# Performance work log

Measured on AMD Instinct MI355X. Metric: run time of the kernel, lower is better.

## Reference

```python
import jax, jax.numpy as jnp
import numpy as np

E, V, F_, B = 8192, 2048, 2048, 8
H, DEC, EDGE, META = 128, 128, 2, 4
MEMH, MEMAGG, AGGH = 256, 128, 128
IN_DIM = DEC + EDGE + META  # 134


def _incidence(idx, n):
    # dense (n, E) 0/1 incidence matrix, as used by torch.mm in the original
    return jnp.zeros((n, idx.shape[0]), jnp.float32).at[idx, jnp.arange(idx.shape[0])].set(1.0)


def setup_inputs() -> dict:
    key = jax.random.key(0)
    ks = jax.random.split(key, 32)
    var_idx = jax.random.randint(ks[0], (E,), 0, V)          # variable of each edge
    fun_idx = jax.random.randint(ks[1], (E,), 0, F_)         # clause of each edge
    batch_of_var = jax.random.randint(ks[2], (V,), 0, B)     # problem id of each variable
    variable_mask = _incidence(var_idx, V)                   # (V, E)
    function_mask = _incidence(fun_idx, F_)                  # (F, E)
    b_variable_mask = jnp.zeros((V, B), jnp.float32).at[jnp.arange(V), batch_of_var].set(1.0)

    def lin(k, i, o):
        kw, kb = jax.random.split(k)
        return (jax.random.normal(kw, (i, o), jnp.float32) * 0.05,
                jax.random.normal(kb, (o,), jnp.float32) * 0.05)

    p = {}
    for pre, k0 in (("v", 10), ("f", 20)):
        p[pre + "M1w"], p[pre + "M1b"] = lin(ks[k0], IN_DIM, MEMH)
        p[pre + "M2w"], p[pre + "M2b"] = lin(ks[k0 + 1], MEMH, MEMAGG)
        p[pre + "A1w"], p[pre + "A1b"] = lin(ks[k0 + 2], MEMAGG + EDGE, AGGH)
        p[pre + "A2w"], p[pre + "A2b"] = lin(ks[k0 + 3], AGGH, H)

    return dict(
        variable_state=jax.random.normal(ks[3], (E, H), jnp.float32),
        function_state=jax.random.normal(ks[4], (E, H), jnp.float32),
        decimator_variable_state=jax.random.normal(ks[5], (E, DEC), jnp.float32),
        decimator_function_state=jax.random.normal(ks[6], (E, DEC), jnp.float32),
        edge_feature=jax.random.normal(ks[7], (E, EDGE), jnp.float32),
        meta_data=jax.random.normal(ks[8], (B, META), jnp.float32),
        active_mask=jax.random.randint(ks[9], (B, 1), 0, 2),
        variable_mask=variable_mask, variable_mask_t=variable_mask.T,
        function_mask=function_mask, function_mask_t=function_mask.T,
        b_variable_mask=b_variable_mask,
        **p,
    )


def _aggregate(state, feature, mask, mask_t, W1, b1, W2, b2, A1, c1, A2, c2):
    # MessageAggregator (include_self_message=False, edge_mask=None)
    h = jax.nn.relu(state @ W1 + b1)       # (E, MEMH)  pre-aggregation transform
    h = h @ W2 + b2                        # (E, MEMAGG)
    agg = mask_t @ (mask @ h) - h          # node-sum broadcast back to edges, minus self message
    a = jax.nn.relu(jnp.concatenate([agg, feature], 1) @ A1 + c1)  # post-agg transform
    return a @ A2 + c2                     # (E, H)


def reference(variable_state, function_state, decimator_variable_state,
              decimator_function_state, edge_feature, meta_data, active_mask,
              variable_mask, variable_mask_t, function_mask, function_mask_t,
              b_variable_mask,
              vM1w, vM1b, vM2w, vM2b, vA1w, vA1b, vA2w, vA2b,
              fM1w, fM1b, fM2w, fM2b, fA1w, fA1b, fA2w, fA2b):
    # active mask broadcast: batch -> variables -> edges (dense mm chain as in torch)
    mask = variable_mask_t @ (b_variable_mask @ active_mask.astype(jnp.float32))  # (E, 1)
    # meta-data broadcast: batch -> variables -> edges
    graph_feat = variable_mask_t @ (b_variable_mask @ meta_data)                  # (E, META)

    dvs = jnp.concatenate([decimator_variable_state, edge_feature, graph_feat], 1)
    agg_v = _aggregate(dvs, edge_feature, variable_mask, variable_mask_t,
                       vM1w, vM1b, vM2w, vM2b, vA1w, vA1b, vA2w, vA2b)
    function_state = mask * agg_v + (1.0 - mask) * function_state  # dropout: identity (eval)

    dfs = jnp.concatenate([decimator_function_state, edge_feature, graph_feat], 1)
    agg_f = _aggregate(dfs, edge_feature, function_mask, function_mask_t,
                       fM1w, fM1b, fM2w, fM2b, fA1w, fA1b, fA2w, fA2b)
    variable_state = mask * agg_f + (1.0 - mask) * variable_state

    return (variable_state, function_state)
```

## Files before the change

kernel.cpp:

```cpp
#include <hip/hip_runtime.h>

#define E_N 8192
#define V_N 2048
#define F_N 2048
#define B_N 8
#define H_N 128
#define DEC_N 128
#define EDGE_N 2
#define META_N 4
#define IN_DIM 134
#define MEMH 256
#define MEMAGG 128
#define AGGH 128

typedef __attribute__((ext_vector_type(8))) short short8;
typedef __attribute__((ext_vector_type(4))) float f32x4;

__device__ inline unsigned short f2bf(float x) {
    unsigned u = __float_as_uint(x);
    unsigned r = (u + 0x7FFFu + ((u >> 16) & 1u)) >> 16;
    return (unsigned short)r;
}

__device__ inline short8 pack8(float4 u0, float4 u1) {
    short8 s;
    s[0] = (short)f2bf(u0.x); s[1] = (short)f2bf(u0.y);
    s[2] = (short)f2bf(u0.z); s[3] = (short)f2bf(u0.w);
    s[4] = (short)f2bf(u1.x); s[5] = (short)f2bf(u1.y);
    s[6] = (short)f2bf(u1.z); s[7] = (short)f2bf(u1.w);
    return s;
}

__device__ inline int probe4(float4 v, int c, int hit) {
    if (hit < 0) {
        if      (v.x != 0.f) hit = c;
        else if (v.y != 0.f) hit = c + 1;
        else if (v.z != 0.f) hit = c + 2;
        else if (v.w != 0.f) hit = c + 3;
    }
    return hit;
}

struct RDesc { const float* src; unsigned short* dst; int K; int N; int Kp; };
struct PrepArgs {
    const float* vmt; const float* fmt;
    int* vidx; int* fidx;
    const float* bvm; const int* active; const float* meta;
    float* emask; float* gfeat;
    float* nszero;
    RDesc d[8];
};
__constant__ const int RP_CUM[9] = {0, 160, 288, 368, 432, 592, 720, 800, 864};

__global__ __launch_bounds__(256) void k_prep(PrepArgs P) {
    int bid = blockIdx.x, tid = threadIdx.x;
    if (bid < 4096) {
        int row = bid * 4 + (tid >> 6);
        int lane = tid & 63;
        bool isVar = row < E_N;
        const float* m = isVar ? P.vmt : P.fmt;
        int* out = isVar ? P.vidx : P.fidx;
        int e = isVar ? row : row - E_N;
        const float4* rp = (const float4*)(m + (size_t)e * V_N);

        int hit = -1;
        float4 a0 = rp[lane], a1 = rp[64 + lane];
        hit = probe4(a0, lane * 4, hit);
        hit = probe4(a1, (64 + lane) * 4, hit);
        unsigned long long bm = __ballot(hit >= 0);
        for (int base = 128; base < 512 && !bm; base += 128) {
            float4 v0 = rp[base + lane], v1 = rp[base + 64 + lane];
            hit = probe4(v0, (base + lane) * 4, hit);
            hit = probe4(v1, (base + 64 + lane) * 4, hit);
            bm = __ballot(hit >= 0);
        }
        int pos = __shfl(hit, __ffsll((long long)bm) - 1);
        if (lane == 0) {
            out[e] = pos;
            if (isVar) {
                const float4* bv = (const float4*)(P.bvm + pos * 8);
                float4 x0 = bv[0], x1 = bv[1];
                float s = x0.y + 2.f * x0.z + 3.f * x0.w +
                          4.f * x1.x + 5.f * x1.y + 6.f * x1.z + 7.f * x1.w;
                int b = (int)(s + 0.5f);
                P.emask[e] = (float)P.active[b];
                ((float4*)P.gfeat)[e] = ((const float4*)P.meta)[b];
            }
        }
        return;
    }
    if (bid < 4608) {
        int gid = (bid - 4096) * 256 + tid;
        ((float4*)P.nszero)[gid] = (float4){0.f, 0.f, 0.f, 0.f};
        return;
    }
    int rb = bid - 4608;
    int mi = 0;
#pragma unroll
    for (int t = 1; t < 8; ++t) if (rb >= RP_CUM[t]) mi = t;
    RDesc d = P.d[mi];
    int i = (rb - RP_CUM[mi]) * 256 + tid;
    if (i >= d.Kp * d.N) return;
    int elem = i & 7;
    int lane = (i >> 3) & 63;
    int f    = i >> 9;
    int c16n = d.N >> 4;
    int c16 = f % c16n, kc = f / c16n;
    int k = kc * 32 + (lane >> 4) * 8 + elem;
    int c = c16 * 16 + (lane & 15);
    float v = (k < d.K) ? d.src[(size_t)k * d.N + c] : 0.f;
    d.dst[i] = f2bf(v);
}

struct F1Args {
    const float* dec[2];
    const float* ef;
    const float* gfeat;
    const unsigned short* wpack[2];
    const float* b1[2];
    const float* b2[2];
    const int* idx[2];
    float* h2[2];
    float* ns[2];
};

__global__ __launch_bounds__(256, 6) void k_fused1(F1Args A) {
    int br = blockIdx.y;
    const float* dec = A.dec[br];
    const unsigned short* W1f = A.wpack[br];
    const unsigned short* W2f = A.wpack[br] + 160 * 256;
    const float* b1 = A.b1[br];
    const float* b2 = A.b2[br];
    const int* idx = A.idx[br];
    float* h2o = A.h2[br];
    float* ns  = A.ns[br];

    int tid = threadIdx.x;
    int wave = tid >> 6, lane = tid & 63;
    int lrow = lane & 15, lgrp = lane >> 4;
    int e0 = blockIdx.x * 16;

    __shared__ unsigned short h1s[16 * 256];

    int n0 = wave * 64;
    f32x4 acc1[4];
#pragma unroll
    for (int nt = 0; nt < 4; ++nt) {
        float bv = b1[n0 + nt * 16 + lrow];
        acc1[nt] = (f32x4){bv, bv, bv, bv};
    }
    const float4* dec4 = (const float4*)dec;
    int r = e0 + lrow;
#pragma unroll
    for (int kc = 0; kc < 5; ++kc) {
        short8 a;
        if (kc < 4) {
            float4 u0 = dec4[(size_t)r * 32 + kc * 8 + lgrp * 2];
            float4 u1 = dec4[(size_t)r * 32 + kc * 8 + lgrp * 2 + 1];
            a = pack8(u0, u1);
        } else {
            short8 z = (short8)0;
            if (lgrp == 0) {
                z[0] = (short)f2bf(A.ef[r * 2]);
                z[1] = (short)f2bf(A.ef[r * 2 + 1]);
                z[2] = (short)f2bf(A.gfeat[r * 4]);
                z[3] = (short)f2bf(A.gfeat[r * 4 + 1]);
                z[4] = (short)f2bf(A.gfeat[r * 4 + 2]);
                z[5] = (short)f2bf(A.gfeat[r * 4 + 3]);
            }
            a = z;
        }
#pragma unroll
        for (int nt = 0; nt < 4; ++nt) {
            short8 b = *(const short8*)(W1f + ((size_t)(kc * 16 + (n0 >> 4) + nt) * 64 + lane) * 8);
            acc1[nt] = __builtin_amdgcn_mfma_f32_16x16x32_bf16(a, b, acc1[nt], 0, 0, 0);
        }
    }
#pragma unroll
    for (int nt = 0; nt < 4; ++nt)
#pragma unroll
        for (int j = 0; j < 4; ++j) {
            int row = lgrp * 4 + j;
            int col = n0 + nt * 16 + lrow;
            h1s[row * 256 + (col ^ ((row & 7) << 3))] = f2bf(fmaxf(acc1[nt][j], 0.f));
        }
    __syncthreads();

    int c0 = wave * 32;
    f32x4 acc2[2];
#pragma unroll
    for (int nt = 0; nt < 2; ++nt) {
        float bv = b2[c0 + nt * 16 + lrow];
        acc2[nt] = (f32x4){bv, bv, bv, bv};
    }
#pragma unroll
    for (int kc = 0; kc < 8; ++kc) {
        int kb = kc * 32 + lgrp * 8;
        short8 a2 = *(const short8*)(h1s + lrow * 256 + (kb ^ ((lrow & 7) << 3)));
#pragma unroll
        for (int nt = 0; nt < 2; ++nt) {
            short8 b = *(const short8*)(W2f + ((size_t)(kc * 8 + (c0 >> 4) + nt) * 64 + lane) * 8);
            acc2[nt] = __builtin_amdgcn_mfma_f32_16x16x32_bf16(a2, b, acc2[nt], 0, 0, 0);
        }
    }
#pragma unroll
    for (int j = 0; j < 4; ++j) {
        int row = e0 + lgrp * 4 + j;
        int node = idx[row];
#pragma unroll
        for (int nt = 0; nt < 2; ++nt) {
            int col = c0 + nt * 16 + lrow;
            float v = acc2[nt][j];
            h2o[(size_t)row * 128 + col] = v;
            atomicAdd(ns + (size_t)node * 128 + col, v);
        }
    }
}

struct F2Args {
    const unsigned short* wpack[2];
    const float* c1[2];
    const float* c2[2];
    const float* h2[2];
    const float* ns[2];
    const int* idx[2];
    const float* ef;
    const float* emask;
    const float* oldst[2];
    float* outst[2];
};

__global__ __launch_bounds__(256, 6) void k_fused2(F2Args A) {
    int br = blockIdx.y;
    const unsigned short* A1f = A.wpack[br] + 160 * 256 + 256 * 128;
    const unsigned short* A2f = A1f + 160 * 128;
    const float* c1 = A.c1[br];
    const float* c2 = A.c2[br];
    const float* h2 = A.h2[br];
    const float* ns = A.ns[br];
    const int* idx = A.idx[br];
    const float* oldst = A.oldst[br];
    float* outst = A.outst[br];

    int tid = threadIdx.x;
    int wave = tid >> 6, lane = tid & 63;
    int lrow = lane & 15, lgrp = lane >> 4;
    int e0 = blockIdx.x * 16;

    __shared__ unsigned short as_[16 * 128];

    int n0 = wave * 32;
    f32x4 accp[2];
#pragma unroll
    for (int nt = 0; nt < 2; ++nt) {
        float bv = c1[n0 + nt * 16 + lrow];
        accp[nt] = (f32x4){bv, bv, bv, bv};
    }
    const float4* ns4 = (const float4*)ns;
    const float4* h24 = (const float4*)h2;
    int r = e0 + lrow;
    int node = idx[r];
#pragma unroll
    for (int kc = 0; kc < 5; ++kc) {
        short8 a;
        if (kc < 4) {
            float4 u0 = ns4[(size_t)node * 32 + kc * 8 + lgrp * 2];
            float4 u1 = ns4[(size_t)node * 32 + kc * 8 + lgrp * 2 + 1];
            float4 v0 = h24[(size_t)r * 32 + kc * 8 + lgrp * 2];
            float4 v1 = h24[(size_t)r * 32 + kc * 8 + lgrp * 2 + 1];
            float4 d0 = {u0.x - v0.x, u0.y - v0.y, u0.z - v0.z, u0.w - v0.w};
            float4 d1 = {u1.x - v1.x, u1.y - v1.y, u1.z - v1.z, u1.w - v1.w};
            a = pack8(d0, d1);
        } else {
            short8 z = (short8)0;
            if (lgrp == 0) {
                z[0] = (short)f2bf(A.ef[r * 2]);
                z[1] = (short)f2bf(A.ef[r * 2 + 1]);
            }
            a = z;
        }
#pragma unroll
        for (int nt = 0; nt < 2; ++nt) {
            short8 b = *(const short8*)(A1f + ((size_t)(kc * 8 + (n0 >> 4) + nt) * 64 + lane) * 8);
            accp[nt] = __builtin_amdgcn_mfma_f32_16x16x32_bf16(a, b, accp[nt], 0, 0, 0);
        }
    }
#pragma unroll
    for (int nt = 0; nt < 2; ++nt)
#pragma unroll
        for (int j = 0; j < 4; ++j) {
            int row = lgrp * 4 + j;
            int col = n0 + nt * 16 + lrow;
            as_[row * 128 + (col ^ ((row & 7) << 3))] = f2bf(fmaxf(accp[nt][j], 0.f));
        }
    __syncthreads();

    f32x4 acco[2];
#pragma unroll
    for (int nt = 0; nt < 2; ++nt) {
        float bv = c2[n0 + nt * 16 + lrow];
        acco[nt] = (f32x4){bv, bv, bv, bv};
    }
#pragma unroll
    for (int kc = 0; kc < 4; ++kc) {
        int kb = kc * 32 + lgrp * 8;
        short8 a2 = *(const short8*)(as_ + lrow * 128 + (kb ^ ((lrow & 7) << 3)));
#pragma unroll
        for (int nt = 0; nt < 2; ++nt) {
            short8 b = *(const short8*)(A2f + ((size_t)(kc * 8 + (n0 >> 4) + nt) * 64 + lane) * 8);
            acco[nt] = __builtin_amdgcn_mfma_f32_16x16x32_bf16(a2, b, acco[nt], 0, 0, 0);
        }
    }
#pragma unroll
    for (int j = 0; j < 4; ++j) {
        int row = e0 + lgrp * 4 + j;
        float m = A.emask[row];
#pragma unroll
        for (int nt = 0; nt < 2; ++nt) {
            int col = n0 + nt * 16 + lrow;
            float old = oldst[(size_t)row * 128 + col];
            outst[(size_t)row * 128 + col] = m * acco[nt][j] + (1.f - m) * old;
        }
    }
}

extern "C" void kernel_launch(void* const* d_in, const int* in_sizes, int n_in,
                              void* d_out, int out_size, void* d_ws, size_t ws_size,
                              hipStream_t stream) {
    const float* variable_state = (const float*)d_in[0];
    const float* function_state = (const float*)d_in[1];
    const float* dec_v          = (const float*)d_in[2];
    const float* dec_f          = (const float*)d_in[3];
    const float* ef             = (const float*)d_in[4];
    const float* meta           = (const float*)d_in[5];
    const int*   active         = (const int*)d_in[6];
    const float* vmask_t        = (const float*)d_in[8];
    const float* fmask_t        = (const float*)d_in[10];
    const float* bvm            = (const float*)d_in[11];
    const float* vM1w = (const float*)d_in[12]; const float* vM1b = (const float*)d_in[13];
    const float* vM2w = (const float*)d_in[14]; const float* vM2b = (const float*)d_in[15];
    const float* vA1w = (const float*)d_in[16]; const float* vA1b = (const float*)d_in[17];
    const float* vA2w = (const float*)d_in[18]; const float* vA2b = (const float*)d_in[19];
    const float* fM1w = (const float*)d_in[20]; const float* fM1b = (const float*)d_in[21];
    const float* fM2w = (const float*)d_in[22]; const float* fM2b = (const float*)d_in[23];
    const float* fA1w = (const float*)d_in[24]; const float* fA1b = (const float*)d_in[25];
    const float* fA2w = (const float*)d_in[26]; const float* fA2b = (const float*)d_in[27];

    float* out_vs = (float*)d_out;
    float* out_fs = (float*)d_out + (size_t)E_N * H_N;

    int*   var_idx = (int*)d_ws;
    int*   fun_idx = var_idx + E_N;
    float* emask   = (float*)(fun_idx + E_N);
    float* gfeat   = emask + E_N;
    float* hv2     = gfeat + (size_t)E_N * 4;
    float* hf2     = hv2 + (size_t)E_N * MEMAGG;
    float* nsv     = hf2 + (size_t)E_N * MEMAGG;
    float* nsf     = nsv + (size_t)V_N * MEMAGG;
    unsigned short* wpack = (unsigned short*)(nsf + (size_t)F_N * MEMAGG);
    const int PBR = 160 * 256 + 256 * 128 + 160 * 128 + 128 * 128;
    unsigned short* wpv = wpack;
    unsigned short* wpf = wpack + PBR;

    PrepArgs pp;
    pp.vmt = vmask_t; pp.fmt = fmask_t;
    pp.vidx = var_idx; pp.fidx = fun_idx;
    pp.bvm = bvm; pp.active = active; pp.meta = meta;
    pp.emask = emask; pp.gfeat = gfeat;
    pp.nszero = nsv;
    pp.d[0] = {vM1w, wpv,                          IN_DIM, MEMH,   160};
    pp.d[1] = {vM2w, wpv + 160 * 256,              MEMH,   MEMAGG, 256};
    pp.d[2] = {vA1w, wpv + 160 * 256 + 256 * 128,  130,    AGGH,   160};
    pp.d[3] = {vA2w, wpv + 160 * 256 + 256 * 128 + 160 * 128, 128, H_N, 128};
    pp.d[4] = {fM1w, wpf,                          IN_DIM, MEMH,   160};
    pp.d[5] = {fM2w, wpf + 160 * 256,              MEMH,   MEMAGG, 256};
    pp.d[6] = {fA1w, wpf + 160 * 256 + 256 * 128,  130,    AGGH,   160};
    pp.d[7] = {fA2w, wpf + 160 * 256 + 256 * 128 + 160 * 128, 128, H_N, 128};
    k_prep<<<5472, 256, 0, stream>>>(pp);

    F1Args f1;
    f1.dec[0] = dec_v;  f1.dec[1] = dec_f;
    f1.ef = ef;         f1.gfeat = gfeat;
    f1.wpack[0] = wpv;  f1.wpack[1] = wpf;
    f1.b1[0] = vM1b;    f1.b1[1] = fM1b;
    f1.b2[0] = vM2b;    f1.b2[1] = fM2b;
    f1.idx[0] = var_idx; f1.idx[1] = fun_idx;
    f1.h2[0] = hv2;     f1.h2[1] = hf2;
    f1.ns[0] = nsv;     f1.ns[1] = nsf;
    k_fused1<<<dim3(E_N / 16, 2), 256, 0, stream>>>(f1);

    F2Args f2;
    f2.wpack[0] = wpv;  f2.wpack[1] = wpf;
    f2.c1[0] = vA1b;    f2.c1[1] = fA1b;
    f2.c2[0] = vA2b;    f2.c2[1] = fA2b;
    f2.h2[0] = hv2;     f2.h2[1] = hf2;
    f2.ns[0] = nsv;     f2.ns[1] = nsf;
    f2.idx[0] = var_idx; f2.idx[1] = fun_idx;
    f2.ef = ef;         f2.emask = emask;
    f2.oldst[0] = function_state;  f2.oldst[1] = variable_state;
    f2.outst[0] = out_fs;          f2.outst[1] = out_vs;
    k_fused2<<<dim3(E_N / 16, 2), 256, 0, stream>>>(f2);
}
```

Baseline: 53.22 us.

## Fold M2 weights into A1 to drop a GEMM from the second kernel

Precomputes M2w·A1w (and b2·A1w) in the prep kernel, so the first kernel directly produces the A1-projected messages and scatters them. The second kernel then only needs a per-edge elementwise combine (node sum minus own, edge-feature term, bias, ReLU) before the final A2 GEMM, removing one MFMA stage and its shared-memory round trip. The cost is a small 128-deep dot-product loop per packed weight element in prep. Rounding the fused weights to bf16 changes numerics slightly.

```diff
diff --git a/kernel.cpp b/kernel.cpp
--- a/kernel.cpp
+++ b/kernel.cpp
@@ -41,16 +41,19 @@
     return hit;
 }
 
-struct RDesc { const float* src; unsigned short* dst; int K; int N; int Kp; };
+struct RDesc { const float* src; const float* src2; unsigned short* dst; int K; int N; int Kp; };
 struct PrepArgs {
     const float* vmt; const float* fmt;
     int* vidx; int* fidx;
     const float* bvm; const int* active; const float* meta;
     float* emask; float* gfeat;
     float* nszero;
-    RDesc d[8];
+    const float* vM2b; const float* fM2b;
+    const float* vA1w; const float* fA1w;
+    float* b2A;
+    RDesc d[6];
 };
-__constant__ const int RP_CUM[9] = {0, 160, 288, 368, 432, 592, 720, 800, 864};
+__constant__ const int RP_CUM[7] = {0, 160, 288, 352, 512, 640, 704};
 
 __global__ __launch_bounds__(256) void k_prep(PrepArgs P) {
     int bid = blockIdx.x, tid = threadIdx.x;
@@ -94,10 +97,20 @@
         ((float4*)P.nszero)[gid] = (float4){0.f, 0.f, 0.f, 0.f};
         return;
     }
+    if (bid == 5312) {
+        int n = tid & 127;
+        const float* b2 = (tid < 128) ? P.vM2b : P.fM2b;
+        const float* A1 = (tid < 128) ? P.vA1w : P.fA1w;
+        float acc = 0.f;
+#pragma unroll 8
+        for (int j = 0; j < 128; ++j) acc += b2[j] * A1[(size_t)j * 128 + n];
+        P.b2A[tid] = acc;
+        return;
+    }
     int rb = bid - 4608;
     int mi = 0;
 #pragma unroll
-    for (int t = 1; t < 8; ++t) if (rb >= RP_CUM[t]) mi = t;
+    for (int t = 1; t < 6; ++t) if (rb >= RP_CUM[t]) mi = t;
     RDesc d = P.d[mi];
     int i = (rb - RP_CUM[mi]) * 256 + tid;
     if (i >= d.Kp * d.N) return;
@@ -108,7 +121,16 @@
     int c16 = f % c16n, kc = f / c16n;
     int k = kc * 32 + (lane >> 4) * 8 + elem;
     int c = c16 * 16 + (lane & 15);
-    float v = (k < d.K) ? d.src[(size_t)k * d.N + c] : 0.f;
+    float v;
+    if (d.src2) {
+        float acc = 0.f;
+#pragma unroll 8
+        for (int j = 0; j < 128; ++j)
+            acc += d.src[(size_t)k * 128 + j] * d.src2[(size_t)j * 128 + c];
+        v = acc;
+    } else {
+        v = (k < d.K) ? d.src[(size_t)k * d.N + c] : 0.f;
+    }
     d.dst[i] = f2bf(v);
 }
 
@@ -118,9 +140,9 @@
     const float* gfeat;
     const unsigned short* wpack[2];
     const float* b1[2];
-    const float* b2[2];
+    const float* b2A[2];
     const int* idx[2];
-    float* h2[2];
+    float* qb[2];
     float* ns[2];
 };
 
@@ -130,9 +152,9 @@
     const unsigned short* W1f = A.wpack[br];
     const unsigned short* W2f = A.wpack[br] + 160 * 256;
     const float* b1 = A.b1[br];
-    const float* b2 = A.b2[br];
+    const float* b2A = A.b2A[br];
     const int* idx = A.idx[br];
-    float* h2o = A.h2[br];
+    float* qbo = A.qb[br];
     float* ns  = A.ns[br];
 
     int tid = threadIdx.x;
@@ -190,7 +212,7 @@
     f32x4 acc2[2];
 #pragma unroll
     for (int nt = 0; nt < 2; ++nt) {
-        float bv = b2[c0 + nt * 16 + lrow];
+        float bv = b2A[c0 + nt * 16 + lrow];
         acc2[nt] = (f32x4){bv, bv, bv, bv};
     }
 #pragma unroll
@@ -211,7 +233,7 @@
         for (int nt = 0; nt < 2; ++nt) {
             int col = c0 + nt * 16 + lrow;
             float v = acc2[nt][j];
-            h2o[(size_t)row * 128 + col] = v;
+            qbo[(size_t)row * 128 + col] = v;
             atomicAdd(ns + (size_t)node * 128 + col, v);
         }
     }
@@ -219,9 +241,10 @@
 
 struct F2Args {
     const unsigned short* wpack[2];
+    const float* a1[2];
     const float* c1[2];
     const float* c2[2];
-    const float* h2[2];
+    const float* qb[2];
     const float* ns[2];
     const int* idx[2];
     const float* ef;
@@ -232,11 +255,12 @@
 
 __global__ __launch_bounds__(256, 6) void k_fused2(F2Args A) {
     int br = blockIdx.y;
-    const unsigned short* A1f = A.wpack[br] + 160 * 256 + 256 * 128;
-    const unsigned short* A2f = A1f + 160 * 128;
+    const unsigned short* A2f = A.wpack[br] + 73728;
+    const float* A1e0 = A.a1[br] + 128 * 128;
+    const float* A1e1 = A.a1[br] + 129 * 128;
     const float* c1 = A.c1[br];
     const float* c2 = A.c2[br];
-    const float* h2 = A.h2[br];
+    const float* qb = A.qb[br];
     const float* ns = A.ns[br];
     const int* idx = A.idx[br];
     const float* oldst = A.oldst[br];
@@ -246,55 +270,14 @@
     int wave = tid >> 6, lane = tid & 63;
     int lrow = lane & 15, lgrp = lane >> 4;
     int e0 = blockIdx.x * 16;
-
-    __shared__ unsigned short as_[16 * 128];
-
-    int n0 = wave * 32;
-    f32x4 accp[2];
-#pragma unroll
-    for (int nt = 0; nt < 2; ++nt) {
-        float bv = c1[n0 + nt * 16 + lrow];
-        accp[nt] = (f32x4){bv, bv, bv, bv};
-    }
-    const float4* ns4 = (const float4*)ns;
-    const float4* h24 = (const float4*)h2;
     int r = e0 + lrow;
     int node = idx[r];
-#pragma unroll
-    for (int kc = 0; kc < 5; ++kc) {
-        short8 a;
-        if (kc < 4) {
-            float4 u0 = ns4[(size_t)node * 32 + kc * 8 + lgrp * 2];
-            float4 u1 = ns4[(size_t)node * 32 + kc * 8 + lgrp * 2 + 1];
-            float4 v0 = h24[(size_t)r * 32 + kc * 8 + lgrp * 2];
-            float4 v1 = h24[(size_t)r * 32 + kc * 8 + lgrp * 2 + 1];
-            float4 d0 = {u0.x - v0.x, u0.y - v0.y, u0.z - v0.z, u0.w - v0.w};
-            float4 d1 = {u1.x - v1.x, u1.y - v1.y, u1.z - v1.z, u1.w - v1.w};
-            a = pack8(d0, d1);
-        } else {
-            short8 z = (short8)0;
-            if (lgrp == 0) {
-                z[0] = (short)f2bf(A.ef[r * 2]);
-                z[1] = (short)f2bf(A.ef[r * 2 + 1]);
-            }
-            a = z;
-        }
-#pragma unroll
-        for (int nt = 0; nt < 2; ++nt) {
-            short8 b = *(const short8*)(A1f + ((size_t)(kc * 8 + (n0 >> 4) + nt) * 64 + lane) * 8);
-            accp[nt] = __builtin_amdgcn_mfma_f32_16x16x32_bf16(a, b, accp[nt], 0, 0, 0);
-        }
-    }
-#pragma unroll
-    for (int nt = 0; nt < 2; ++nt)
-#pragma unroll
-        for (int j = 0; j < 4; ++j) {
-            int row = lgrp * 4 + j;
-            int col = n0 + nt * 16 + lrow;
-            as_[row * 128 + (col ^ ((row & 7) << 3))] = f2bf(fmaxf(accp[nt][j], 0.f));
-        }
-    __syncthreads();
-
+    float ef0 = A.ef[r * 2], ef1 = A.ef[r * 2 + 1];
+
+    const float4* ns4 = (const float4*)(ns + (size_t)node * 128);
+    const float4* qb4 = (const float4*)(qb + (size_t)r * 128);
+
+    int n0 = wave * 32;
     f32x4 acco[2];
 #pragma unroll
     for (int nt = 0; nt < 2; ++nt) {
@@ -303,12 +286,25 @@
     }
 #pragma unroll
     for (int kc = 0; kc < 4; ++kc) {
-        int kb = kc * 32 + lgrp * 8;
-        short8 a2 = *(const short8*)(as_ + lrow * 128 + (kb ^ ((lrow & 7) << 3)));
+        int k0 = kc * 32 + lgrp * 8;
+        float4 u0 = ns4[k0 >> 2],       u1 = ns4[(k0 >> 2) + 1];
+        float4 q0 = qb4[k0 >> 2],       q1 = qb4[(k0 >> 2) + 1];
+        float4 w00 = *(const float4*)(A1e0 + k0), w01 = *(const float4*)(A1e0 + k0 + 4);
+        float4 w10 = *(const float4*)(A1e1 + k0), w11 = *(const float4*)(A1e1 + k0 + 4);
+        float4 cc0 = *(const float4*)(c1 + k0),   cc1 = *(const float4*)(c1 + k0 + 4);
+        short8 a;
+        a[0] = (short)f2bf(fmaxf(u0.x - q0.x + ef0 * w00.x + ef1 * w10.x + cc0.x, 0.f));
+        a[1] = (short)f2bf(fmaxf(u0.y - q0.y + ef0 * w00.y + ef1 * w10.y + cc0.y, 0.f));
+        a[2] = (short)f2bf(fmaxf(u0.z - q0.z + ef0 * w00.z + ef1 * w10.z + cc0.z, 0.f));
+        a[3] = (short)f2bf(fmaxf(u0.w - q0.w + ef0 * w00.w + ef1 * w10.w + cc0.w, 0.f));
+        a[4] = (short)f2bf(fmaxf(u1.x - q1.x + ef0 * w01.x + ef1 * w11.x + cc1.x, 0.f));
+        a[5] = (short)f2bf(fmaxf(u1.y - q1.y + ef0 * w01.y + ef1 * w11.y + cc1.y, 0.f));
+        a[6] = (short)f2bf(fmaxf(u1.z - q1.z + ef0 * w01.z + ef1 * w11.z + cc1.z, 0.f));
+        a[7] = (short)f2bf(fmaxf(u1.w - q1.w + ef0 * w01.w + ef1 * w11.w + cc1.w, 0.f));
 #pragma unroll
         for (int nt = 0; nt < 2; ++nt) {
             short8 b = *(const short8*)(A2f + ((size_t)(kc * 8 + (n0 >> 4) + nt) * 64 + lane) * 8);
-            acco[nt] = __builtin_amdgcn_mfma_f32_16x16x32_bf16(a2, b, acco[nt], 0, 0, 0);
+            acco[nt] = __builtin_amdgcn_mfma_f32_16x16x32_bf16(a, b, acco[nt], 0, 0, 0);
         }
     }
 #pragma unroll
@@ -353,12 +349,13 @@
     int*   fun_idx = var_idx + E_N;
     float* emask   = (float*)(fun_idx + E_N);
     float* gfeat   = emask + E_N;
-    float* hv2     = gfeat + (size_t)E_N * 4;
-    float* hf2     = hv2 + (size_t)E_N * MEMAGG;
-    float* nsv     = hf2 + (size_t)E_N * MEMAGG;
+    float* qv      = gfeat + (size_t)E_N * 4;
+    float* qf      = qv + (size_t)E_N * MEMAGG;
+    float* nsv     = qf + (size_t)E_N * MEMAGG;
     float* nsf     = nsv + (size_t)V_N * MEMAGG;
-    unsigned short* wpack = (unsigned short*)(nsf + (size_t)F_N * MEMAGG);
-    const int PBR = 160 * 256 + 256 * 128 + 160 * 128 + 128 * 128;
+    float* b2A     = nsf + (size_t)F_N * MEMAGG;
+    unsigned short* wpack = (unsigned short*)(b2A + 256);
+    const int PBR = 40960 + 32768 + 16384;
     unsigned short* wpv = wpack;
     unsigned short* wpf = wpack + PBR;
 
@@ -368,32 +365,34 @@
     pp.bvm = bvm; pp.active = active; pp.meta = meta;
     pp.emask = emask; pp.gfeat = gfeat;
     pp.nszero = nsv;
-    pp.d[0] = {vM1w, wpv,                          IN_DIM, MEMH,   160};
-    pp.d[1] = {vM2w, wpv + 160 * 256,              MEMH,   MEMAGG, 256};
-    pp.d[2] = {vA1w, wpv + 160 * 256 + 256 * 128,  130,    AGGH,   160};
-    pp.d[3] = {vA2w, wpv + 160 * 256 + 256 * 128 + 160 * 128, 128, H_N, 128};
-    pp.d[4] = {fM1w, wpf,                          IN_DIM, MEMH,   160};
-    pp.d[5] = {fM2w, wpf + 160 * 256,              MEMH,   MEMAGG, 256};
-    pp.d[6] = {fA1w, wpf + 160 * 256 + 256 * 128,  130,    AGGH,   160};
-    pp.d[7] = {fA2w, wpf + 160 * 256 + 256 * 128 + 160 * 128, 128, H_N, 128};
-    k_prep<<<5472, 256, 0, stream>>>(pp);
+    pp.vM2b = vM2b; pp.fM2b = fM2b;
+    pp.vA1w = vA1w; pp.fA1w = fA1w;
+    pp.b2A = b2A;
+    pp.d[0] = {vM1w, nullptr, wpv,                 IN_DIM, MEMH,   160};
+    pp.d[1] = {vM2w, vA1w,    wpv + 40960,         MEMH,   MEMAGG, 256};
+    pp.d[2] = {vA2w, nullptr, wpv + 73728,         128,    H_N,    128};
+    pp.d[3] = {fM1w, nullptr, wpf,                 IN_DIM, MEMH,   160};
+    pp.d[4] = {fM2w, fA1w,    wpf + 40960,         MEMH,   MEMAGG, 256};
+    pp.d[5] = {fA2w, nullptr, wpf + 73728,         128,    H_N,    128};
+    k_prep<<<5313, 256, 0, stream>>>(pp);
 
     F1Args f1;
     f1.dec[0] = dec_v;  f1.dec[1] = dec_f;
     f1.ef = ef;         f1.gfeat = gfeat;
     f1.wpack[0] = wpv;  f1.wpack[1] = wpf;
     f1.b1[0] = vM1b;    f1.b1[1] = fM1b;
-    f1.b2[0] = vM2b;    f1.b2[1] = fM2b;
+    f1.b2A[0] = b2A;    f1.b2A[1] = b2A + 128;
     f1.idx[0] = var_idx; f1.idx[1] = fun_idx;
-    f1.h2[0] = hv2;     f1.h2[1] = hf2;
+    f1.qb[0] = qv;      f1.qb[1] = qf;
     f1.ns[0] = nsv;     f1.ns[1] = nsf;
     k_fused1<<<dim3(E_N / 16, 2), 256, 0, stream>>>(f1);
 
     F2Args f2;
     f2.wpack[0] = wpv;  f2.wpack[1] = wpf;
+    f2.a1[0] = vA1w;    f2.a1[1] = fA1w;
     f2.c1[0] = vA1b;    f2.c1[1] = fA1b;
     f2.c2[0] = vA2b;    f2.c2[1] = fA2b;
-    f2.h2[0] = hv2;     f2.h2[1] = hf2;
+    f2.qb[0] = qv;      f2.qb[1] = qf;
     f2.ns[0] = nsv;     f2.ns[1] = nsf;
     f2.idx[0] = var_idx; f2.idx[1] = fun_idx;
     f2.ef = ef;         f2.emask = emask;
```

After: 67.53 us. +26.9%, slower.
